# Optimization experiments

Measured on AMD Instinct MI355X. Metric: run time of the kernel, lower is better.

## Reference

```python
import jax, jax.numpy as jnp
import numpy as np

H = 1.0  # RBF bandwidth (init kwarg h)


def setup_inputs() -> dict:
    key = jax.random.key(0)
    k1, k2 = jax.random.split(key)
    x = jax.random.normal(k1, (8192, 512), dtype=jnp.float32)
    x1 = jax.random.normal(k2, (8192, 512), dtype=jnp.float32)
    return {"x": x, "x1": x1}


def reference(x, x1):
    # exp(-||x_i - x1_j||^2 / h), computed via the GEMM trick to avoid the
    # O(N*M*D) broadcast intermediate the original torch code materializes.
    x_sq = jnp.sum(x * x, axis=-1, keepdims=True)          # [N, 1]
    x1_sq = jnp.sum(x1 * x1, axis=-1)                       # [M]
    cross = jnp.einsum('nd,md->nm', x, x1)                  # [N, M]
    d = jnp.maximum(x_sq + x1_sq[None, :] - 2.0 * cross, 0.0)
    return jnp.exp(-d / H)
```

## Files before the change

kernel.cpp:

```cpp
#include <hip/hip_runtime.h>
#include <stdint.h>
#include <stddef.h>


#define NROWS 8192
#define DIMK  512

typedef __bf16 bf16x8 __attribute__((ext_vector_type(8)));
typedef int    i32x8  __attribute__((ext_vector_type(8)));
typedef int    i32x4  __attribute__((ext_vector_type(4)));
typedef float  f32x4  __attribute__((ext_vector_type(4)));

#define AS1 __attribute__((address_space(1)))
#define AS3 __attribute__((address_space(3)))

#define WAITV(n) asm volatile("s_waitcnt vmcnt(" #n ")" ::: "memory")
#define WAITL()  asm volatile("s_waitcnt lgkmcnt(0)" ::: "memory")
#define BAR()    asm volatile("s_barrier" ::: "memory")

__device__ __forceinline__ uint32_t f2bf(float f) {
    uint32_t u = __float_as_uint(f);
    return (u + 0x7FFFu + ((u >> 16) & 1u)) >> 16;
}

__device__ __forceinline__ uint32_t pk_fp8x4(float a, float b, float c, float d) {
    int w = __builtin_amdgcn_cvt_pk_fp8_f32(a, b, 0, false);
    w     = __builtin_amdgcn_cvt_pk_fp8_f32(c, d, w, true);
    return (uint32_t)w;
}

__device__ __forceinline__ i32x8 ld_frag(const uint8_t* base, int c_lo, int c_hi) {
    i32x4 lo = *(const i32x4*)(base + c_lo);
    i32x4 hi = *(const i32x4*)(base + c_hi);
    i32x8 r;
    r[0] = lo[0]; r[1] = lo[1]; r[2] = lo[2]; r[3] = lo[3];
    r[4] = hi[0]; r[5] = hi[1]; r[6] = hi[2]; r[7] = hi[3];
    return r;
}

__global__ __launch_bounds__(256) void precast_fp8(
    const float* __restrict__ x, const float* __restrict__ x1,
    uint8_t* __restrict__ xf, uint8_t* __restrict__ x1f,
    float* __restrict__ xsq, float* __restrict__ x1sq)
{
    const int w    = threadIdx.x >> 6;
    const int lane = threadIdx.x & 63;
    const int row  = blockIdx.x * 4 + w;
    const float* src;
    uint8_t* dstb;
    float* dsts;
    if (blockIdx.y == 0) { src = x  + (size_t)row * DIMK; dstb = xf  + (size_t)row * DIMK; dsts = xsq  + row; }
    else                 { src = x1 + (size_t)row * DIMK; dstb = x1f + (size_t)row * DIMK; dsts = x1sq + row; }

    float4 v0 = ((const float4*)src)[lane * 2];
    float4 v1 = ((const float4*)src)[lane * 2 + 1];
    float s = v0.x * v0.x + v0.y * v0.y + v0.z * v0.z + v0.w * v0.w
            + v1.x * v1.x + v1.y * v1.y + v1.z * v1.z + v1.w * v1.w;

    uint2 p;
    p.x = pk_fp8x4(v0.x, v0.y, v0.z, v0.w);
    p.y = pk_fp8x4(v1.x, v1.y, v1.z, v1.w);
    ((uint2*)dstb)[lane] = p;

    #pragma unroll
    for (int off = 32; off > 0; off >>= 1) s += __shfl_down(s, off);
    if (lane == 0) *dsts = s;
}

__global__ __launch_bounds__(256) void norms_only(
    const float* __restrict__ x, const float* __restrict__ x1,
    float* __restrict__ xsq, float* __restrict__ x1sq)
{
    const int row = blockIdx.x;
    const float* src = (blockIdx.y == 0) ? x + (size_t)row * DIMK : x1 + (size_t)row * DIMK;
    float* dsts      = (blockIdx.y == 0) ? xsq + row : x1sq + row;
    const int t = threadIdx.x;
    float2 v = ((const float2*)src)[t];
    float s = v.x * v.x + v.y * v.y;
    #pragma unroll
    for (int off = 32; off > 0; off >>= 1) s += __shfl_down(s, off);
    __shared__ float red[4];
    if ((t & 63) == 0) red[t >> 6] = s;
    __syncthreads();
    if (t == 0) *dsts = red[0] + red[1] + red[2] + red[3];
}

__global__ __launch_bounds__(256) void rbf_pers_mxfp8(
    const uint8_t* __restrict__ Xf, const uint8_t* __restrict__ X1f,
    const float* __restrict__ xsq, const float* __restrict__ x1sq,
    float* __restrict__ out)
{
    __shared__ uint8_t lds[81920];

    const int t    = threadIdx.x;
    const int id   = blockIdx.x;
    const int xcd  = id & 7;
    const int loc  = id >> 3;
    const int rp   = (xcd << 4) | (loc & 15);
    const int cq   = loc >> 4;
    const int lane = t & 63;
    const int w    = t >> 6;
    const int wm   = w >> 1;
    const int wn   = w & 1;

    const int lrow = lane & 15;
    const int q    = lane >> 4;
    const int s    = lrow & 7;
    const int c_lo = ((2 * q)     ^ s) * 16;
    const int c_hi = ((2 * q + 1) ^ s) * 16;

    {
        const uint8_t* gA = Xf + (size_t)rp * 64 * DIMK;
        #pragma unroll
        for (int c = 0; c < 8; ++c) {
            const int g   = c * 256 + t;
            const int r   = g >> 5;
            const int off = r * DIMK + ((g & 24) << 4) + (((g & 7) ^ (r & 7)) << 4);
            __builtin_amdgcn_global_load_lds((AS1 void*)(gA + off),
                                             (AS3 void*)(&lds[(size_t)g * 16]), 16, 0, 0);
        }
    }

    i32x4 breg[8];
    {
        const uint8_t* gB = X1f + (size_t)(cq * 32 + 0) * 64 * DIMK;
        #pragma unroll
        for (int c = 0; c < 8; ++c)
            breg[c] = *(const i32x4*)(gB + (size_t)(c * 256 + t) * 16);
    }

    float xsl[2];
    #pragma unroll
    for (int fi = 0; fi < 2; ++fi)
        xsl[fi] = xsq[rp * 64 + wm * 32 + fi * 16 + lrow];

    f32x4 x1n[2];
    #pragma unroll
    for (int fj = 0; fj < 2; ++fj)
        x1n[fj] = *(const f32x4*)&x1sq[(cq * 32 + 0) * 64 + wn * 32 + fj * 16 + q * 4];

    uint8_t* scr = &lds[65536 + w * 4096];
    const int crow = lane >> 3;
    const int clc  = lane & 7;

    #pragma unroll 1
    for (int i = 0; i < 32; ++i) {
        BAR();
        WAITV(2);

        f32x4 x1v0 = x1n[0], x1v1 = x1n[1];

        #pragma unroll
        for (int c = 0; c < 8; ++c) {
            const int g   = c * 256 + t;
            const int r   = g >> 5;
            const int dst = 32768 + r * DIMK + ((g & 24) << 4) + (((g & 7) ^ (r & 7)) << 4);
            *(i32x4*)(&lds[dst]) = breg[c];
        }
        WAITL(); BAR();

        {
            const int ip = (i < 31) ? i + 1 : 31;
            const uint8_t* gB = X1f + (size_t)(cq * 32 + ip) * 64 * DIMK;
            #pragma unroll
            for (int c = 0; c < 8; ++c)
                breg[c] = *(const i32x4*)(gB + (size_t)(c * 256 + t) * 16);
            #pragma unroll
            for (int fj = 0; fj < 2; ++fj)
                x1n[fj] = *(const f32x4*)&x1sq[(cq * 32 + ip) * 64 + wn * 32 + fj * 16 + q * 4];
        }

        f32x4 acc[2][2];
        #pragma unroll
        for (int a = 0; a < 2; ++a)
            #pragma unroll
            for (int b = 0; b < 2; ++b)
                acc[a][b] = f32x4{0.f, 0.f, 0.f, 0.f};

        #pragma unroll
        for (int kt = 0; kt < 4; ++kt) {
            i32x8 af[2], bg[2];
            #pragma unroll
            for (int fi = 0; fi < 2; ++fi)
                af[fi] = ld_frag(&lds[(wm * 32 + fi * 16 + lrow) * DIMK + kt * 128], c_lo, c_hi);
            #pragma unroll
            for (int fj = 0; fj < 2; ++fj)
                bg[fj] = ld_frag(&lds[32768 + (wn * 32 + fj * 16 + lrow) * DIMK + kt * 128], c_lo, c_hi);
            #pragma unroll
            for (int fj = 0; fj < 2; ++fj)
                #pragma unroll
                for (int fi = 0; fi < 2; ++fi)
                    acc[fj][fi] = __builtin_amdgcn_mfma_scale_f32_16x16x128_f8f6f4(
                        bg[fj], af[fi], acc[fj][fi],
                        0, 0, 0, 0x7F7F7F7F, 0, 0x7F7F7F7F);
        }

        #pragma unroll
        for (int fi = 0; fi < 2; ++fi)
            #pragma unroll
            for (int fj = 0; fj < 2; ++fj) {
                f32x4 a  = acc[fj][fi];
                f32x4 x1v = (fj == 0) ? x1v0 : x1v1;
                f32x4 ev;
                #pragma unroll
                for (int r = 0; r < 4; ++r) {
                    float d = fmaxf(xsl[fi] + x1v[r] - 2.0f * a[r], 0.0f);
                    ev[r] = __expf(-d);
                }
                const int rl = fi * 16 + lrow;
                const int lc = fj * 4 + q;
                *(f32x4*)(scr + rl * 128 + ((lc ^ (rl & 7)) * 16)) = ev;
            }
        {
            float* gbase = out + (size_t)(rp * 64 + wm * 32) * NROWS
                               + (size_t)(cq * 32 + i) * 64 + wn * 32;
            #pragma unroll
            for (int si = 0; si < 4; ++si) {
                const int row = si * 8 + crow;
                f32x4 v = *(const f32x4*)(scr + row * 128 + ((clc ^ (row & 7)) * 16));
                __builtin_nontemporal_store(v, (f32x4*)(gbase + (size_t)row * NROWS + clc * 4));
            }
        }
    }
}

#define FBM 128
#define FBN 128
__global__ __launch_bounds__(256) void rbf_mfma_inline(
    const float* __restrict__ X, const float* __restrict__ X1,
    const float* __restrict__ xsq, const float* __restrict__ x1sq,
    float* __restrict__ out)
{
    __shared__ uint16_t As[FBM * 32];
    __shared__ uint16_t Bs[FBN * 32];

    const int t    = threadIdx.x;
    const int bm   = blockIdx.x;
    const int bn   = blockIdx.y;
    const int lane = t & 63;
    const int w    = t >> 6;
    const int wm   = w >> 1;
    const int wn   = w & 1;

    f32x4 acc[4][4];
    #pragma unroll
    for (int i = 0; i < 4; ++i)
        #pragma unroll
        for (int j = 0; j < 4; ++j)
            acc[i][j] = f32x4{0.f, 0.f, 0.f, 0.f};

    const int lrow = lane & 15;
    const int kq   = (lane >> 4) * 8;
    int aoff[4], boff[4];
    #pragma unroll
    for (int i = 0; i < 4; ++i) {
        aoff[i] = (wm * 64 + i * 16 + lrow) * 32 + kq;
        boff[i] = (wn * 64 + i * 16 + lrow) * 32 + kq;
    }

    #pragma unroll 1
    for (int kt = 0; kt < DIMK / 32; ++kt) {
        #pragma unroll
        for (int i = 0; i < 4; ++i) {
            const int g   = t + i * 256;
            const int row = g >> 3;
            const int c4  = (g & 7) * 4;
            float4 va = *(const float4*)&X [(size_t)(bm * FBM + row) * DIMK + kt * 32 + c4];
            float4 vb = *(const float4*)&X1[(size_t)(bn * FBN + row) * DIMK + kt * 32 + c4];
            uint2 pa, pb;
            pa.x = f2bf(va.x) | (f2bf(va.y) << 16);
            pa.y = f2bf(va.z) | (f2bf(va.w) << 16);
            pb.x = f2bf(vb.x) | (f2bf(vb.y) << 16);
            pb.y = f2bf(vb.z) | (f2bf(vb.w) << 16);
            *(uint2*)&As[g * 4] = pa;
            *(uint2*)&Bs[g * 4] = pb;
        }
        __syncthreads();

        bf16x8 af[4], bg[4];
        #pragma unroll
        for (int i = 0; i < 4; ++i) af[i] = *(const bf16x8*)&As[aoff[i]];
        #pragma unroll
        for (int i = 0; i < 4; ++i) bg[i] = *(const bf16x8*)&Bs[boff[i]];
        #pragma unroll
        for (int i = 0; i < 4; ++i)
            #pragma unroll
            for (int j = 0; j < 4; ++j)
                acc[i][j] = __builtin_amdgcn_mfma_f32_16x16x32_bf16(af[i], bg[j], acc[i][j], 0, 0, 0);
        __syncthreads();
    }

    const int row0 = bm * FBM + wm * 64 + (lane >> 4) * 4;
    const int col0 = bn * FBN + wn * 64 + lrow;
    float xs[4][4], x1s[4];
    #pragma unroll
    for (int tm = 0; tm < 4; ++tm)
        #pragma unroll
        for (int r = 0; r < 4; ++r) xs[tm][r] = xsq[row0 + tm * 16 + r];
    #pragma unroll
    for (int tn = 0; tn < 4; ++tn) x1s[tn] = x1sq[col0 + tn * 16];

    #pragma unroll
    for (int tm = 0; tm < 4; ++tm)
        #pragma unroll
        for (int tn = 0; tn < 4; ++tn)
            #pragma unroll
            for (int r = 0; r < 4; ++r) {
                const int row = row0 + tm * 16 + r;
                const int col = col0 + tn * 16;
                float d = xs[tm][r] + x1s[tn] - 2.0f * acc[tm][tn][r];
                d = fmaxf(d, 0.0f);
                out[(size_t)row * NROWS + col] = __expf(-d);
            }
}

extern "C" void kernel_launch(void* const* d_in, const int* in_sizes, int n_in,
                              void* d_out, int out_size, void* d_ws, size_t ws_size,
                              hipStream_t stream)
{
    const float* x  = (const float*)d_in[0];
    const float* x1 = (const float*)d_in[1];
    float* out = (float*)d_out;

    const size_t f8_bytes  = (size_t)NROWS * DIMK;
    const size_t need_full = 2 * f8_bytes + 2 * (size_t)NROWS * sizeof(float);

    if (ws_size >= need_full) {
        uint8_t* xf   = (uint8_t*)d_ws;
        uint8_t* x1f  = xf + f8_bytes;
        float*   xsq  = (float*)((char*)d_ws + 2 * f8_bytes);
        float*   x1sq = xsq + NROWS;
        precast_fp8<<<dim3(NROWS / 4, 2), 256, 0, stream>>>(x, x1, xf, x1f, xsq, x1sq);
        rbf_pers_mxfp8<<<512, 256, 0, stream>>>(xf, x1f, xsq, x1sq, out);
    } else {
        float* xsq  = (float*)d_ws;
        float* x1sq = xsq + NROWS;
        norms_only<<<dim3(NROWS, 2), 256, 0, stream>>>(x, x1, xsq, x1sq);
        rbf_mfma_inline<<<dim3(NROWS / FBM, NROWS / FBN), 256, 0, stream>>>(x, x1, xsq, x1sq, out);
    }
}
```

Baseline: 326.4 us.

## Restructure fp8 RBF kernel into 16-row blocks streaming B fragments from global

Replaces the persistent 64x64-tile kernel (LDS-staged A and B, double-buffered B prefetch) with a 512-block kernel where each block owns 16 full output rows. A fragments are held in registers and B fragments are loaded directly from global/L2 with no LDS staging. Output is written through a 64KB LDS slab so each row is stored as contiguous 4KB segments. This drops the LDS staging and barriers for B and makes stores fully row-contiguous, but each block rereads all of X1 from cache and loses the explicit prefetch overlap.

```diff
diff --git a/kernel.cpp b/kernel.cpp
--- a/kernel.cpp
+++ b/kernel.cpp
@@ -11,13 +11,6 @@
 typedef int    i32x4  __attribute__((ext_vector_type(4)));
 typedef float  f32x4  __attribute__((ext_vector_type(4)));
 
-#define AS1 __attribute__((address_space(1)))
-#define AS3 __attribute__((address_space(3)))
-
-#define WAITV(n) asm volatile("s_waitcnt vmcnt(" #n ")" ::: "memory")
-#define WAITL()  asm volatile("s_waitcnt lgkmcnt(0)" ::: "memory")
-#define BAR()    asm volatile("s_barrier" ::: "memory")
-
 __device__ __forceinline__ uint32_t f2bf(float f) {
     uint32_t u = __float_as_uint(f);
     return (u + 0x7FFFu + ((u >> 16) & 1u)) >> 16;
@@ -27,15 +20,6 @@
     int w = __builtin_amdgcn_cvt_pk_fp8_f32(a, b, 0, false);
     w     = __builtin_amdgcn_cvt_pk_fp8_f32(c, d, w, true);
     return (uint32_t)w;
-}
-
-__device__ __forceinline__ i32x8 ld_frag(const uint8_t* base, int c_lo, int c_hi) {
-    i32x4 lo = *(const i32x4*)(base + c_lo);
-    i32x4 hi = *(const i32x4*)(base + c_hi);
-    i32x8 r;
-    r[0] = lo[0]; r[1] = lo[1]; r[2] = lo[2]; r[3] = lo[3];
-    r[4] = hi[0]; r[5] = hi[1]; r[6] = hi[2]; r[7] = hi[3];
-    return r;
 }
 
 __global__ __launch_bounds__(256) void precast_fp8(
@@ -85,142 +69,88 @@
     if (t == 0) *dsts = red[0] + red[1] + red[2] + red[3];
 }
 
-__global__ __launch_bounds__(256) void rbf_pers_mxfp8(
+__global__ __launch_bounds__(512, 4) void rbf_rows_mxfp8(
     const uint8_t* __restrict__ Xf, const uint8_t* __restrict__ X1f,
     const float* __restrict__ xsq, const float* __restrict__ x1sq,
     float* __restrict__ out)
 {
-    __shared__ uint8_t lds[81920];
+    __shared__ uint8_t slab[65536];
 
     const int t    = threadIdx.x;
     const int id   = blockIdx.x;
-    const int xcd  = id & 7;
-    const int loc  = id >> 3;
-    const int rp   = (xcd << 4) | (loc & 15);
-    const int cq   = loc >> 4;
     const int lane = t & 63;
     const int w    = t >> 6;
-    const int wm   = w >> 1;
-    const int wn   = w & 1;
-
     const int lrow = lane & 15;
     const int q    = lane >> 4;
-    const int s    = lrow & 7;
-    const int c_lo = ((2 * q)     ^ s) * 16;
-    const int c_hi = ((2 * q + 1) ^ s) * 16;
-
-    {
-        const uint8_t* gA = Xf + (size_t)rp * 64 * DIMK;
-        #pragma unroll
-        for (int c = 0; c < 8; ++c) {
-            const int g   = c * 256 + t;
-            const int r   = g >> 5;
-            const int off = r * DIMK + ((g & 24) << 4) + (((g & 7) ^ (r & 7)) << 4);
-            __builtin_amdgcn_global_load_lds((AS1 void*)(gA + off),
-                                             (AS3 void*)(&lds[(size_t)g * 16]), 16, 0, 0);
-        }
-    }
-
-    i32x4 breg[8];
-    {
-        const uint8_t* gB = X1f + (size_t)(cq * 32 + 0) * 64 * DIMK;
-        #pragma unroll
-        for (int c = 0; c < 8; ++c)
-            breg[c] = *(const i32x4*)(gB + (size_t)(c * 256 + t) * 16);
-    }
-
-    float xsl[2];
-    #pragma unroll
-    for (int fi = 0; fi < 2; ++fi)
-        xsl[fi] = xsq[rp * 64 + wm * 32 + fi * 16 + lrow];
-
-    f32x4 x1n[2];
-    #pragma unroll
-    for (int fj = 0; fj < 2; ++fj)
-        x1n[fj] = *(const f32x4*)&x1sq[(cq * 32 + 0) * 64 + wn * 32 + fj * 16 + q * 4];
-
-    uint8_t* scr = &lds[65536 + w * 4096];
-    const int crow = lane >> 3;
-    const int clc  = lane & 7;
+
+    const uint8_t* gA = Xf + (size_t)(id * 16 + lrow) * DIMK + q * 32;
+    i32x8 af[4];
+    #pragma unroll
+    for (int kt = 0; kt < 4; ++kt)
+        af[kt] = *(const i32x8*)(gA + kt * 128);
+
+    const float xr = xsq[id * 16 + lrow];
 
     #pragma unroll 1
-    for (int i = 0; i < 32; ++i) {
-        BAR();
-        WAITV(2);
-
-        f32x4 x1v0 = x1n[0], x1v1 = x1n[1];
-
-        #pragma unroll
-        for (int c = 0; c < 8; ++c) {
-            const int g   = c * 256 + t;
-            const int r   = g >> 5;
-            const int dst = 32768 + r * DIMK + ((g & 24) << 4) + (((g & 7) ^ (r & 7)) << 4);
-            *(i32x4*)(&lds[dst]) = breg[c];
-        }
-        WAITL(); BAR();
-
-        {
-            const int ip = (i < 31) ? i + 1 : 31;
-            const uint8_t* gB = X1f + (size_t)(cq * 32 + ip) * 64 * DIMK;
-            #pragma unroll
-            for (int c = 0; c < 8; ++c)
-                breg[c] = *(const i32x4*)(gB + (size_t)(c * 256 + t) * 16);
-            #pragma unroll
-            for (int fj = 0; fj < 2; ++fj)
-                x1n[fj] = *(const f32x4*)&x1sq[(cq * 32 + ip) * 64 + wn * 32 + fj * 16 + q * 4];
-        }
-
-        f32x4 acc[2][2];
-        #pragma unroll
-        for (int a = 0; a < 2; ++a)
-            #pragma unroll
-            for (int b = 0; b < 2; ++b)
-                acc[a][b] = f32x4{0.f, 0.f, 0.f, 0.f};
-
-        #pragma unroll
-        for (int kt = 0; kt < 4; ++kt) {
-            i32x8 af[2], bg[2];
-            #pragma unroll
-            for (int fi = 0; fi < 2; ++fi)
-                af[fi] = ld_frag(&lds[(wm * 32 + fi * 16 + lrow) * DIMK + kt * 128], c_lo, c_hi);
-            #pragma unroll
-            for (int fj = 0; fj < 2; ++fj)
-                bg[fj] = ld_frag(&lds[32768 + (wn * 32 + fj * 16 + lrow) * DIMK + kt * 128], c_lo, c_hi);
-            #pragma unroll
-            for (int fj = 0; fj < 2; ++fj)
+    for (int sl = 0; sl < 8; ++sl) {
+        f32x4 acc[2][4];
+        #pragma unroll
+        for (int u = 0; u < 2; ++u)
+            #pragma unroll
+            for (int fj = 0; fj < 4; ++fj)
+                acc[u][fj] = f32x4{0.f, 0.f, 0.f, 0.f};
+
+        #pragma unroll
+        for (int u = 0; u < 2; ++u) {
+            const int bt = sl * 16 + w + u * 8;
+            const uint8_t* gB = X1f + (size_t)(bt * 64 + lrow) * DIMK + q * 32;
+            #pragma unroll
+            for (int kt = 0; kt < 4; ++kt) {
+                i32x8 bg[4];
                 #pragma unroll
-                for (int fi = 0; fi < 2; ++fi)
-                    acc[fj][fi] = __builtin_amdgcn_mfma_scale_f32_16x16x128_f8f6f4(
-                        bg[fj], af[fi], acc[fj][fi],
+                for (int fj = 0; fj < 4; ++fj)
+                    bg[fj] = *(const i32x8*)(gB + (size_t)fj * 16 * DIMK + kt * 128);
+                #pragma unroll
+                for (int fj = 0; fj < 4; ++fj)
+                    acc[u][fj] = __builtin_amdgcn_mfma_scale_f32_16x16x128_f8f6f4(
+                        bg[fj], af[kt], acc[u][fj],
                         0, 0, 0, 0x7F7F7F7F, 0, 0x7F7F7F7F);
-        }
-
-        #pragma unroll
-        for (int fi = 0; fi < 2; ++fi)
-            #pragma unroll
-            for (int fj = 0; fj < 2; ++fj) {
-                f32x4 a  = acc[fj][fi];
-                f32x4 x1v = (fj == 0) ? x1v0 : x1v1;
+            }
+        }
+
+        #pragma unroll
+        for (int u = 0; u < 2; ++u) {
+            const int bt = sl * 16 + w + u * 8;
+            #pragma unroll
+            for (int fj = 0; fj < 4; ++fj) {
+                f32x4 x1v = *(const f32x4*)&x1sq[bt * 64 + fj * 16 + q * 4];
+                f32x4 a = acc[u][fj];
                 f32x4 ev;
                 #pragma unroll
                 for (int r = 0; r < 4; ++r) {
-                    float d = fmaxf(xsl[fi] + x1v[r] - 2.0f * a[r], 0.0f);
+                    float d = fmaxf(xr + x1v[r] - 2.0f * a[r], 0.0f);
                     ev[r] = __expf(-d);
                 }
-                const int rl = fi * 16 + lrow;
-                const int lc = fj * 4 + q;
-                *(f32x4*)(scr + rl * 128 + ((lc ^ (rl & 7)) * 16)) = ev;
-            }
-        {
-            float* gbase = out + (size_t)(rp * 64 + wm * 32) * NROWS
-                               + (size_t)(cq * 32 + i) * 64 + wn * 32;
-            #pragma unroll
-            for (int si = 0; si < 4; ++si) {
-                const int row = si * 8 + crow;
-                f32x4 v = *(const f32x4*)(scr + row * 128 + ((clc ^ (row & 7)) * 16));
-                __builtin_nontemporal_store(v, (f32x4*)(gbase + (size_t)row * NROWS + clc * 4));
-            }
-        }
+                const int c  = (w + u * 8) * 16 + fj * 4 + q;
+                const int cs = (c & ~7) | ((c & 7) ^ (lrow & 7));
+                *(f32x4*)(&slab[lrow * 4096 + cs * 16]) = ev;
+            }
+        }
+        __syncthreads();
+
+        #pragma unroll
+        for (int sr = 0; sr < 2; ++sr) {
+            const int row = w * 2 + sr;
+            float* gbase = out + (size_t)(id * 16 + row) * NROWS + sl * 1024;
+            #pragma unroll
+            for (int k = 0; k < 4; ++k) {
+                const int cc = k * 64 + lane;
+                const int cs = (cc & ~7) | ((cc & 7) ^ (row & 7));
+                f32x4 v = *(const f32x4*)(&slab[row * 4096 + cs * 16]);
+                __builtin_nontemporal_store(v, (f32x4*)(gbase + cc * 4));
+            }
+        }
+        __syncthreads();
     }
 }
 
@@ -331,7 +261,7 @@
         float*   xsq  = (float*)((char*)d_ws + 2 * f8_bytes);
         float*   x1sq = xsq + NROWS;
         precast_fp8<<<dim3(NROWS / 4, 2), 256, 0, stream>>>(x, x1, xf, x1f, xsq, x1sq);
-        rbf_pers_mxfp8<<<512, 256, 0, stream>>>(xf, x1f, xsq, x1sq, out);
+        rbf_rows_mxfp8<<<NROWS / 16, 512, 0, stream>>>(xf, x1f, xsq, x1sq, out);
     } else {
         float* xsq  = (float*)d_ws;
         float* x1sq = xsq + NROWS;
```

Measured after the change: 494.4 us. 1.51x slower.
